# Optimization experiments

Hardware: AMD Instinct MI355X
Metric: run time of the kernel (lower is better)

Reference implementation:

```python
import jax, jax.numpy as jnp
import numpy as np

B, L, HID, H = 2, 384, 512, 8
D = HID // H  # head_dim = 64


def setup_inputs() -> dict:
    key = jax.random.key(0)
    ks = jax.random.split(key, 16)
    s = 0.02
    return {
        "query": jax.random.normal(ks[0], (B, L, HID), jnp.float32),
        "key_": jax.random.normal(ks[1], (B, L, HID), jnp.float32),
        "value": jax.random.normal(ks[2], (B, L, HID), jnp.float32),
        "mask": jnp.ones((B, 1, 1, L), jnp.int32),
        # fc_q/k/v/o: nn.Linear(hid_dim, hid_dim)
        "Wq": jax.random.normal(ks[3], (HID, HID), jnp.float32) * s,
        "bq": jnp.zeros((HID,), jnp.float32),
        "Wk": jax.random.normal(ks[4], (HID, HID), jnp.float32) * s,
        "bk": jnp.zeros((HID,), jnp.float32),
        "Wv": jax.random.normal(ks[5], (HID, HID), jnp.float32) * s,
        "bv": jnp.zeros((HID,), jnp.float32),
        "Wo": jax.random.normal(ks[6], (HID, HID), jnp.float32) * s,
        "bo": jnp.zeros((HID,), jnp.float32),
        # additive-attention score MLP: W1, W2: Linear(D, D); v: Linear(D, 1)
        "W1": jax.random.normal(ks[7], (D, D), jnp.float32) * s,
        "b1": jnp.zeros((D,), jnp.float32),
        "W2": jax.random.normal(ks[8], (D, D), jnp.float32) * s,
        "b2": jnp.zeros((D,), jnp.float32),
        "vw": jax.random.normal(ks[9], (1, D), jnp.float32) * s,
        "vb": jnp.zeros((1,), jnp.float32),
    }


def reference(query, key_, value, mask, Wq, bq, Wk, bk, Wv, bv, Wo, bo,
              W1, b1, W2, b2, vw, vb):
    b = query.shape[0]
    # projections (torch Linear: x @ W.T + b)
    Q = query @ Wq.T + bq
    K = key_ @ Wk.T + bk
    V = value @ Wv.T + bv
    # [b, h, l, d]
    def split_heads(x):
        return x.reshape(b, -1, H, D).transpose(0, 2, 1, 3)
    Q, K, V = split_heads(Q), split_heads(K), split_heads(V)
    # additive (Bahdanau-style) score: v^T tanh(W1 q + W2 k)
    tQ = Q @ W1.T + b1            # [b, h, lq, d]
    tK = K @ W2.T + b2            # [b, h, lk, d]
    e = jnp.tanh(tQ[:, :, :, None, :] + tK[:, :, None, :, :])  # [b,h,lq,lk,d]
    energy = jnp.einsum('bhqkd,d->bhqk', e, vw[0]) + vb[0]      # [b,h,lq,lk]
    energy = jnp.where(mask == 0, jnp.float32(-1e10), energy)
    attention = jax.nn.softmax(energy, axis=-1)
    x = jnp.einsum('bhqk,bhkd->bhqd', attention, V)  # dropout p=0 (eval)
    x = x.transpose(0, 2, 1, 3).reshape(b, -1, HID)
    x = x @ Wo.T + bo
    return x, attention
```

## Files before the change

### kernel.cpp

```cpp
#include <hip/hip_runtime.h>

#define BATCH 2
#define LSEQ 384
#define NHID 512
#define NH 8
#define DH 64
#define BH (BATCH*NH)
#define XELEMS ((size_t)768 * NHID)
#define TQ 8
#define QTILES (LSEQ/TQ)

typedef unsigned short ushort_t;
typedef __attribute__((ext_vector_type(8))) short bf16x8;
typedef __attribute__((ext_vector_type(4))) float f32x4;

__device__ __forceinline__ float bf2f(ushort_t u) {
    unsigned int v = ((unsigned int)u) << 16;
    return __uint_as_float(v);
}
__device__ __forceinline__ ushort_t f2bf(float f) {
    unsigned int u = __float_as_uint(f);
    unsigned int lsb = (u >> 16) & 1u;
    u += 0x7fffu + lsb;
    return (ushort_t)(u >> 16);
}
__device__ __forceinline__ unsigned pk_bf16(float a, float b) {
    unsigned ua = __float_as_uint(a), ub = __float_as_uint(b);
    ua += 0x7fffu + ((ua >> 16) & 1u);
    ub += 0x7fffu + ((ub >> 16) & 1u);
    return __builtin_amdgcn_perm(ub, ua, 0x07060302);
}
__device__ __forceinline__ float ld1(const void* p, size_t i, int f) {
    return f ? ((const float*)p)[i] : bf2f(((const ushort_t*)p)[i]);
}
__device__ __forceinline__ float4 ld4(const void* p, size_t i, int f) {
    if (f) return ((const float4*)p)[i >> 2];
    ushort4 u = ((const ushort4*)p)[i >> 2];
    return make_float4(bf2f(u.x), bf2f(u.y), bf2f(u.z), bf2f(u.w));
}
__device__ __forceinline__ int block_detect(const unsigned int* q, int* cnt) {
    int t = threadIdx.x;
    if (t == 0) *cnt = 0;
    __syncthreads();
    int n = blockDim.x < 256 ? blockDim.x : 256;
    if (t < n) {
        unsigned int elo = (q[t] >> 7) & 0xFFu;
        if (elo >= 100u && elo <= 150u) atomicAdd(cnt, 1);
    }
    __syncthreads();
    return (*cnt * 2 > n) ? 0 : 1;
}
__device__ __forceinline__ uint4 packu4(float4 a, float4 b) {
    uint4 r;
    r.x = pk_bf16(a.x, a.y); r.y = pk_bf16(a.z, a.w);
    r.z = pk_bf16(b.x, b.y); r.w = pk_bf16(b.z, b.w);
    return r;
}
__device__ __forceinline__ bf16x8 pack_bf8(float4 a, float4 b) {
    union { uint4 u; bf16x8 v; } r;
    r.u = packu4(a, b);
    return r.v;
}

#define OFF_ETQ   16
#define OFF_ETK   (16 + 393216)
#define OFF_VH    (16 + 2*393216)
#define OFF_XH    (16 + 3*393216)

#define LDSTR 72

__global__ __launch_bounds__(128) void gemm_qkv(
    const void* qp, const void* kp, const void* vp,
    const void* Wqp, const void* Wkp, const void* Wvp,
    const void* W1p, const void* W2p,
    const void* bqp, const void* bkp, const void* b1p, const void* b2p,
    const void* bvp, float* __restrict__ ws)
{
    __shared__ int s_cnt;
    __shared__ ushort_t smA[32 * LDSTR];
    __shared__ ushort_t smB[64 * LDSTR];
    __shared__ float biasF[64];
    const int f = block_detect((const unsigned int*)qp, &s_cnt);

    const int mode = blockIdx.z;
    const void* A = (mode == 0) ? qp : (mode == 1) ? kp : vp;
    const void* W = (mode == 0) ? Wqp : (mode == 1) ? Wkp : Wvp;
    const void* W1x = (mode == 1) ? W2p : W1p;

    const int h    = blockIdx.x;
    const int col0 = h * 64;
    const int row0 = blockIdx.y * 32;
    const int t = threadIdx.x;
    const int w = t >> 6, l16 = t & 15, quad = (t & 63) >> 4;

    if (t < 64) {
        if (mode == 2) {
            biasF[t] = ld1(bvp, col0 + t, f);
        } else {
            const void* b1x = (mode == 1) ? b2p : b1p;
            const void* bx  = (mode == 1) ? bkp : bqp;
            float s = ld1(b1x, t, f);
            for (int j = 0; j < 64; j++)
                s = fmaf(ld1(W1x, (size_t)t * 64 + j, f), ld1(bx, h * 64 + j, f), s);
            biasF[t] = s;
        }
    }

    const int arow = t >> 2, acol = (t & 3) * 16;
    const int brow = t >> 1, bcol = (t & 1) * 32;
    const size_t abase = (size_t)(row0 + arow) * 512 + acol;
    const size_t bbase = (size_t)(col0 + brow) * 512 + bcol;

    float4 a4[4], b4[8];
    #pragma unroll
    for (int i = 0; i < 4; i++) a4[i] = ld4(A, abase + i * 4, f);
    #pragma unroll
    for (int i = 0; i < 8; i++) b4[i] = ld4(W, bbase + i * 4, f);

    f32x4 acc[4];
    #pragma unroll
    for (int nt = 0; nt < 4; nt++) acc[nt] = (f32x4){0.f, 0.f, 0.f, 0.f};

    for (int k0 = 0; k0 < 512; k0 += 64) {
        __syncthreads();
        *reinterpret_cast<uint4*>(&smA[arow * LDSTR + acol])     = packu4(a4[0], a4[1]);
        *reinterpret_cast<uint4*>(&smA[arow * LDSTR + acol + 8]) = packu4(a4[2], a4[3]);
        *reinterpret_cast<uint4*>(&smB[brow * LDSTR + bcol])      = packu4(b4[0], b4[1]);
        *reinterpret_cast<uint4*>(&smB[brow * LDSTR + bcol + 8])  = packu4(b4[2], b4[3]);
        *reinterpret_cast<uint4*>(&smB[brow * LDSTR + bcol + 16]) = packu4(b4[4], b4[5]);
        *reinterpret_cast<uint4*>(&smB[brow * LDSTR + bcol + 24]) = packu4(b4[6], b4[7]);
        __syncthreads();
        if (k0 + 64 < 512) {
            #pragma unroll
            for (int i = 0; i < 4; i++) a4[i] = ld4(A, abase + k0 + 64 + i * 4, f);
            #pragma unroll
            for (int i = 0; i < 8; i++) b4[i] = ld4(W, bbase + k0 + 64 + i * 4, f);
        }
        #pragma unroll
        for (int kk = 0; kk < 2; kk++) {
            bf16x8 af = *reinterpret_cast<const bf16x8*>(
                &smA[(w * 16 + l16) * LDSTR + kk * 32 + quad * 8]);
            #pragma unroll
            for (int nt = 0; nt < 4; nt++) {
                bf16x8 bfr = *reinterpret_cast<const bf16x8*>(
                    &smB[(nt * 16 + l16) * LDSTR + kk * 32 + quad * 8]);
                acc[nt] = __builtin_amdgcn_mfma_f32_16x16x32_bf16(af, bfr, acc[nt], 0, 0, 0);
            }
        }
    }

    const int b  = (row0 >= LSEQ) ? 1 : 0;
    const int lbase = row0 - b * LSEQ + w * 16;
    const int bh = b * NH + h;

    if (mode == 2) {
        float* Out = ws + OFF_VH;
        #pragma unroll
        for (int nt = 0; nt < 4; nt++) {
            int d = l16 + nt * 16;
            float bi = biasF[d];
            #pragma unroll
            for (int r = 0; r < 4; r++) {
                int l = lbase + quad * 4 + r;
                Out[(size_t)(bh * LSEQ + l) * 64 + d] = acc[nt][r] + bi;
            }
        }
    } else {
        #pragma unroll
        for (int nt = 0; nt < 4; nt++)
            #pragma unroll
            for (int r = 0; r < 4; r++)
                smA[(w * 16 + quad * 4 + r) * LDSTR + l16 + nt * 16] =
                    f2bf(acc[nt][r]);
        f32x4 acc2[4];
        #pragma unroll
        for (int nt = 0; nt < 4; nt++) acc2[nt] = (f32x4){0.f, 0.f, 0.f, 0.f};
        #pragma unroll
        for (int kk = 0; kk < 2; kk++) {
            bf16x8 af2 = *reinterpret_cast<const bf16x8*>(
                &smA[(w * 16 + l16) * LDSTR + kk * 32 + quad * 8]);
            #pragma unroll
            for (int nt = 0; nt < 4; nt++) {
                int od = nt * 16 + l16, j0 = kk * 32 + quad * 8;
                float4 wa = ld4(W1x, (size_t)od * 64 + j0, f);
                float4 wb = ld4(W1x, (size_t)od * 64 + j0 + 4, f);
                bf16x8 bfw = pack_bf8(wa, wb);
                acc2[nt] = __builtin_amdgcn_mfma_f32_16x16x32_bf16(af2, bfw, acc2[nt], 0, 0, 0);
            }
        }
        float* Out = ws + ((mode == 0) ? OFF_ETQ : OFF_ETK);
        #pragma unroll
        for (int nt = 0; nt < 4; nt++) {
            int d = l16 + nt * 16;
            float bi = biasF[d];
            #pragma unroll
            for (int r = 0; r < 4; r++) {
                int l = lbase + quad * 4 + r;
                Out[(size_t)(bh * LSEQ + l) * 64 + d] =
                    __expf(2.f * (acc2[nt][r] + bi));
            }
        }
    }
}

__global__ __launch_bounds__(384, 6) void attn_kernel(
    const void* qp, const void* vwp, const void* vbp,
    const float* __restrict__ ws_in, float* __restrict__ ws,
    const int* __restrict__ mask, void* __restrict__ dout)
{
    __shared__ int s_cnt;
    const int f = block_detect((const unsigned int*)qp, &s_cnt);

    const float* Etq = ws_in + OFF_ETQ;
    const float* Etk = ws_in + OFF_ETK;
    const float* Vh  = ws_in + OFF_VH;
    float* Xh = ws + OFF_XH;

    const int bid = blockIdx.x;
    const int qt = bid % QTILES;
    const int bh = bid / QTILES;
    const int q0 = qt * TQ;
    const int b  = bh >> 3;
    const int h  = bh & 7;
    const int t  = threadIdx.x;
    const int wave = t >> 6;

    __shared__ __align__(16) float etq8[64][TQ];
    __shared__ float cws[64];
    __shared__ float ps[TQ][LSEQ];
    __shared__ float red[6][TQ][16][4];
    __shared__ float rsum[TQ][6];
    __shared__ float s_vb;

    for (int i = t; i < TQ * 64; i += 384) {
        int qi = i >> 6, d = i & 63;
        float wv = ld1(vwp, d, f);
        etq8[d][qi] = Etq[(size_t)(bh * LSEQ + q0 + qi) * 64 + d] / wv;
    }
    if (t < 64) {
        float v = ld1(vwp, t, f);
        cws[t] = 1.0f / v;
        #pragma unroll
        for (int off = 32; off > 0; off >>= 1) v += __shfl_xor(v, off, 64);
        if (t == 0) s_vb = ld1(vbp, 0, f) + v;
    }
    const int mok = mask[b * LSEQ + t];
    __syncthreads();
    const float vbSum = s_vb;

    float e2[TQ] = {0.f, 0.f, 0.f, 0.f, 0.f, 0.f, 0.f, 0.f};
    const float* ekrow = Etk + (size_t)(bh * LSEQ + t) * 64;
    #pragma unroll 2
    for (int dv = 0; dv < 16; dv++) {
        float4 ek4 = *reinterpret_cast<const float4*>(ekrow + dv * 4);
        #pragma unroll
        for (int pj = 0; pj < 2; pj++) {
            const int d0 = dv * 4 + pj * 2;
            const float ekA = pj ? ek4.z : ek4.x;
            const float ekB = pj ? ek4.w : ek4.y;
            const float cA = cws[d0];
            const float cB = cws[d0 + 1];
            float4 qA0 = *reinterpret_cast<const float4*>(&etq8[d0][0]);
            float4 qA1 = *reinterpret_cast<const float4*>(&etq8[d0][4]);
            float4 qB0 = *reinterpret_cast<const float4*>(&etq8[d0 + 1][0]);
            float4 qB1 = *reinterpret_cast<const float4*>(&etq8[d0 + 1][4]);
            {
                float u1 = fmaf(qA0.x, ekA, cA), u2 = fmaf(qB0.x, ekB, cB);
                e2[0] = fmaf(u1 + u2, __builtin_amdgcn_rcpf(u1 * u2), e2[0]);
            }
            {
                float u1 = fmaf(qA0.y, ekA, cA), u2 = fmaf(qB0.y, ekB, cB);
                e2[1] = fmaf(u1 + u2, __builtin_amdgcn_rcpf(u1 * u2), e2[1]);
            }
            {
                float u1 = fmaf(qA0.z, ekA, cA), u2 = fmaf(qB0.z, ekB, cB);
                e2[2] = fmaf(u1 + u2, __builtin_amdgcn_rcpf(u1 * u2), e2[2]);
            }
            {
                float u1 = fmaf(qA0.w, ekA, cA), u2 = fmaf(qB0.w, ekB, cB);
                e2[3] = fmaf(u1 + u2, __builtin_amdgcn_rcpf(u1 * u2), e2[3]);
            }
            {
                float u1 = fmaf(qA1.x, ekA, cA), u2 = fmaf(qB1.x, ekB, cB);
                e2[4] = fmaf(u1 + u2, __builtin_amdgcn_rcpf(u1 * u2), e2[4]);
            }
            {
                float u1 = fmaf(qA1.y, ekA, cA), u2 = fmaf(qB1.y, ekB, cB);
                e2[5] = fmaf(u1 + u2, __builtin_amdgcn_rcpf(u1 * u2), e2[5]);
            }
            {
                float u1 = fmaf(qA1.z, ekA, cA), u2 = fmaf(qB1.z, ekB, cB);
                e2[6] = fmaf(u1 + u2, __builtin_amdgcn_rcpf(u1 * u2), e2[6]);
            }
            {
                float u1 = fmaf(qA1.w, ekA, cA), u2 = fmaf(qB1.w, ekB, cB);
                e2[7] = fmaf(u1 + u2, __builtin_amdgcn_rcpf(u1 * u2), e2[7]);
            }
        }
    }

    float p[TQ];
    #pragma unroll
    for (int qi = 0; qi < TQ; qi++) {
        float en = fmaf(-2.0f, e2[qi], vbSum);
        if (mok == 0) en = -1e10f;
        p[qi] = __expf(en);
        float s = p[qi];
        #pragma unroll
        for (int off = 32; off > 0; off >>= 1) s += __shfl_xor(s, off, 64);
        if ((t & 63) == 0) rsum[qi][wave] = s;
    }
    __syncthreads();
    #pragma unroll
    for (int qi = 0; qi < TQ; qi++) {
        float gs = rsum[qi][0] + rsum[qi][1] + rsum[qi][2] +
                   rsum[qi][3] + rsum[qi][4] + rsum[qi][5];
        p[qi] *= 1.0f / gs;
        ps[qi][t] = p[qi];
        size_t aidx = XELEMS + (size_t)(bh * LSEQ + q0 + qi) * LSEQ + t;
        if (f) ((float*)dout)[aidx] = p[qi];
        else   ((ushort_t*)dout)[aidx] = f2bf(p[qi]);
    }
    __syncthreads();

    const int dq = t & 15;
    const int ksub = t >> 4;
    const float* vb4 = Vh + (size_t)bh * LSEQ * 64 + dq * 4;
    float4 acc[TQ];
    #pragma unroll
    for (int qi = 0; qi < TQ; qi++) acc[qi] = make_float4(0.f, 0.f, 0.f, 0.f);
    for (int kk = ksub; kk < LSEQ; kk += 24) {
        float4 v4 = *reinterpret_cast<const float4*>(vb4 + (size_t)kk * 64);
        #pragma unroll
        for (int qi = 0; qi < TQ; qi++) {
            float pq = ps[qi][kk];
            acc[qi].x = fmaf(pq, v4.x, acc[qi].x);
            acc[qi].y = fmaf(pq, v4.y, acc[qi].y);
            acc[qi].z = fmaf(pq, v4.z, acc[qi].z);
            acc[qi].w = fmaf(pq, v4.w, acc[qi].w);
        }
    }
    #pragma unroll
    for (int qi = 0; qi < TQ; qi++) {
        #pragma unroll
        for (int off = 16; off <= 32; off <<= 1) {
            acc[qi].x += __shfl_xor(acc[qi].x, off, 64);
            acc[qi].y += __shfl_xor(acc[qi].y, off, 64);
            acc[qi].z += __shfl_xor(acc[qi].z, off, 64);
            acc[qi].w += __shfl_xor(acc[qi].w, off, 64);
        }
    }
    if ((t & 63) < 16) {
        #pragma unroll
        for (int qi = 0; qi < TQ; qi++) {
            red[wave][qi][dq][0] = acc[qi].x;
            red[wave][qi][dq][1] = acc[qi].y;
            red[wave][qi][dq][2] = acc[qi].z;
            red[wave][qi][dq][3] = acc[qi].w;
        }
    }
    __syncthreads();
    if (t < 256) {
        int d = t & 63;
        #pragma unroll
        for (int half = 0; half < 2; half++) {
            int qi = (t >> 6) + half * 4;
            float sx = 0.f;
            #pragma unroll
            for (int w = 0; w < 6; w++) sx += red[w][qi][d >> 2][d & 3];
            Xh[((size_t)(b * LSEQ + q0 + qi) * NH + h) * 64 + d] = sx;
        }
    }
}

__global__ __launch_bounds__(128) void gemm_out(
    const void* qp, const void* Wop, const void* bop,
    const float* __restrict__ ws_in, void* __restrict__ dout)
{
    __shared__ int s_cnt;
    __shared__ ushort_t smA[32 * LDSTR];
    __shared__ ushort_t smB[64 * LDSTR];
    __shared__ float biasF[64];
    const int f = block_detect((const unsigned int*)qp, &s_cnt);

    const float* Xh = ws_in + OFF_XH;
    const int col0 = blockIdx.x * 64;
    const int row0 = blockIdx.y * 32;
    const int t = threadIdx.x;
    const int w = t >> 6, l16 = t & 15, quad = (t & 63) >> 4;

    if (t < 64) biasF[t] = ld1(bop, col0 + t, f);

    const int arow = t >> 2, acol = (t & 3) * 16;
    const int brow = t >> 1, bcol = (t & 1) * 32;
    const float* Ab = Xh + (size_t)(row0 + arow) * 512 + acol;
    const size_t bbase = (size_t)(col0 + brow) * 512 + bcol;

    float4 a4[4], b4[8];
    #pragma unroll
    for (int i = 0; i < 4; i++) a4[i] = *reinterpret_cast<const float4*>(Ab + i * 4);
    #pragma unroll
    for (int i = 0; i < 8; i++) b4[i] = ld4(Wop, bbase + i * 4, f);

    f32x4 acc[4];
    #pragma unroll
    for (int nt = 0; nt < 4; nt++) acc[nt] = (f32x4){0.f, 0.f, 0.f, 0.f};

    for (int k0 = 0; k0 < 512; k0 += 64) {
        __syncthreads();
        *reinterpret_cast<uint4*>(&smA[arow * LDSTR + acol])     = packu4(a4[0], a4[1]);
        *reinterpret_cast<uint4*>(&smA[arow * LDSTR + acol + 8]) = packu4(a4[2], a4[3]);
        *reinterpret_cast<uint4*>(&smB[brow * LDSTR + bcol])      = packu4(b4[0], b4[1]);
        *reinterpret_cast<uint4*>(&smB[brow * LDSTR + bcol + 8])  = packu4(b4[2], b4[3]);
        *reinterpret_cast<uint4*>(&smB[brow * LDSTR + bcol + 16]) = packu4(b4[4], b4[5]);
        *reinterpret_cast<uint4*>(&smB[brow * LDSTR + bcol + 24]) = packu4(b4[6], b4[7]);
        __syncthreads();
        if (k0 + 64 < 512) {
            #pragma unroll
            for (int i = 0; i < 4; i++)
                a4[i] = *reinterpret_cast<const float4*>(Ab + k0 + 64 + i * 4);
            #pragma unroll
            for (int i = 0; i < 8; i++) b4[i] = ld4(Wop, bbase + k0 + 64 + i * 4, f);
        }
        #pragma unroll
        for (int kk = 0; kk < 2; kk++) {
            bf16x8 af = *reinterpret_cast<const bf16x8*>(
                &smA[(w * 16 + l16) * LDSTR + kk * 32 + quad * 8]);
            #pragma unroll
            for (int nt = 0; nt < 4; nt++) {
                bf16x8 bfr = *reinterpret_cast<const bf16x8*>(
                    &smB[(nt * 16 + l16) * LDSTR + kk * 32 + quad * 8]);
                acc[nt] = __builtin_amdgcn_mfma_f32_16x16x32_bf16(af, bfr, acc[nt], 0, 0, 0);
            }
        }
    }

    #pragma unroll
    for (int nt = 0; nt < 4; nt++) {
        int n = col0 + l16 + nt * 16;
        float bi = biasF[l16 + nt * 16];
        #pragma unroll
        for (int r = 0; r < 4; r++) {
            int m = row0 + w * 16 + quad * 4 + r;
            float c = acc[nt][r] + bi;
            size_t idx = (size_t)m * 512 + n;
            if (f) ((float*)dout)[idx] = c;
            else   ((ushort_t*)dout)[idx] = f2bf(c);
        }
    }
}

extern "C" void kernel_launch(void* const* d_in, const int* in_sizes, int n_in,
                              void* d_out, int out_size, void* d_ws, size_t ws_size,
                              hipStream_t stream)
{
    const void* qp = d_in[0];
    const void* kp = d_in[1];
    const void* vp = d_in[2];
    const int* mask = (const int*)d_in[3];
    const void* Wqp = d_in[4];  const void* bqp = d_in[5];
    const void* Wkp = d_in[6];  const void* bkp = d_in[7];
    const void* Wvp = d_in[8];  const void* bvp = d_in[9];
    const void* Wop = d_in[10]; const void* bop = d_in[11];
    const void* W1p = d_in[12]; const void* b1p = d_in[13];
    const void* W2p = d_in[14]; const void* b2p = d_in[15];
    const void* vwp = d_in[16]; const void* vbp = d_in[17];

    float* ws = (float*)d_ws;

    gemm_qkv<<<dim3(8, 24, 3), 128, 0, stream>>>(qp, kp, vp, Wqp, Wkp, Wvp,
                                                 W1p, W2p, bqp, bkp, b1p, b2p,
                                                 bvp, ws);
    attn_kernel<<<BH * QTILES, 384, 0, stream>>>(qp, vwp, vbp, ws, ws, mask, d_out);
    gemm_out<<<dim3(8, 24, 1), 128, 0, stream>>>(qp, Wop, bop, ws, d_out);
}
```

Measured before the change: 159.2 us.

## Split K dimension across two thread halves in projection GEMMs

Both projection GEMM kernels now launch 256 threads per block. Each half handles one half of the K=512 reduction using separate shared-memory tiles, and the two partial accumulators are combined through a shared-memory reduction buffer. The aim is to halve the serial K-loop length and double the waves per block, hiding the global-load latency of these small GEMMs. The cost is more shared memory, an extra reduction sync, and half the threads sitting idle in the epilogue.

```diff
diff --git a/kernel.cpp b/kernel.cpp
--- a/kernel.cpp
+++ b/kernel.cpp
@@ -69,7 +69,7 @@
 
 #define LDSTR 72
 
-__global__ __launch_bounds__(128) void gemm_qkv(
+__global__ __launch_bounds__(256) void gemm_qkv(
     const void* qp, const void* kp, const void* vp,
     const void* Wqp, const void* Wkp, const void* Wvp,
     const void* W1p, const void* W2p,
@@ -77,8 +77,9 @@
     const void* bvp, float* __restrict__ ws)
 {
     __shared__ int s_cnt;
-    __shared__ ushort_t smA[32 * LDSTR];
-    __shared__ ushort_t smB[64 * LDSTR];
+    __shared__ ushort_t smA[2][32 * LDSTR];
+    __shared__ ushort_t smB[2][64 * LDSTR];
+    __shared__ float sred[32][65];
     __shared__ float biasF[64];
     const int f = block_detect((const unsigned int*)qp, &s_cnt);
 
@@ -91,7 +92,10 @@
     const int col0 = h * 64;
     const int row0 = blockIdx.y * 32;
     const int t = threadIdx.x;
-    const int w = t >> 6, l16 = t & 15, quad = (t & 63) >> 4;
+    const int th = t & 127;
+    const int kh = t >> 7;
+    const int w2 = (t >> 6) & 1;
+    const int l16 = t & 15, quad = (t & 63) >> 4;
 
     if (t < 64) {
         if (mode == 2) {
@@ -106,10 +110,10 @@
         }
     }
 
-    const int arow = t >> 2, acol = (t & 3) * 16;
-    const int brow = t >> 1, bcol = (t & 1) * 32;
-    const size_t abase = (size_t)(row0 + arow) * 512 + acol;
-    const size_t bbase = (size_t)(col0 + brow) * 512 + bcol;
+    const int arow = th >> 2, acol = (th & 3) * 16;
+    const int brow = th >> 1, bcol = (th & 1) * 32;
+    const size_t abase = (size_t)(row0 + arow) * 512 + kh * 256 + acol;
+    const size_t bbase = (size_t)(col0 + brow) * 512 + kh * 256 + bcol;
 
     float4 a4[4], b4[8];
     #pragma unroll
@@ -121,16 +125,16 @@
     #pragma unroll
     for (int nt = 0; nt < 4; nt++) acc[nt] = (f32x4){0.f, 0.f, 0.f, 0.f};
 
-    for (int k0 = 0; k0 < 512; k0 += 64) {
+    for (int k0 = 0; k0 < 256; k0 += 64) {
         __syncthreads();
-        *reinterpret_cast<uint4*>(&smA[arow * LDSTR + acol])     = packu4(a4[0], a4[1]);
-        *reinterpret_cast<uint4*>(&smA[arow * LDSTR + acol + 8]) = packu4(a4[2], a4[3]);
-        *reinterpret_cast<uint4*>(&smB[brow * LDSTR + bcol])      = packu4(b4[0], b4[1]);
-        *reinterpret_cast<uint4*>(&smB[brow * LDSTR + bcol + 8])  = packu4(b4[2], b4[3]);
-        *reinterpret_cast<uint4*>(&smB[brow * LDSTR + bcol + 16]) = packu4(b4[4], b4[5]);
-        *reinterpret_cast<uint4*>(&smB[brow * LDSTR + bcol + 24]) = packu4(b4[6], b4[7]);
+        *reinterpret_cast<uint4*>(&smA[kh][arow * LDSTR + acol])     = packu4(a4[0], a4[1]);
+        *reinterpret_cast<uint4*>(&smA[kh][arow * LDSTR + acol + 8]) = packu4(a4[2], a4[3]);
+        *reinterpret_cast<uint4*>(&smB[kh][brow * LDSTR + bcol])      = packu4(b4[0], b4[1]);
+        *reinterpret_cast<uint4*>(&smB[kh][brow * LDSTR + bcol + 8])  = packu4(b4[2], b4[3]);
+        *reinterpret_cast<uint4*>(&smB[kh][brow * LDSTR + bcol + 16]) = packu4(b4[4], b4[5]);
+        *reinterpret_cast<uint4*>(&smB[kh][brow * LDSTR + bcol + 24]) = packu4(b4[6], b4[7]);
         __syncthreads();
-        if (k0 + 64 < 512) {
+        if (k0 + 64 < 256) {
             #pragma unroll
             for (int i = 0; i < 4; i++) a4[i] = ld4(A, abase + k0 + 64 + i * 4, f);
             #pragma unroll
@@ -139,65 +143,81 @@
         #pragma unroll
         for (int kk = 0; kk < 2; kk++) {
             bf16x8 af = *reinterpret_cast<const bf16x8*>(
-                &smA[(w * 16 + l16) * LDSTR + kk * 32 + quad * 8]);
+                &smA[kh][(w2 * 16 + l16) * LDSTR + kk * 32 + quad * 8]);
             #pragma unroll
             for (int nt = 0; nt < 4; nt++) {
                 bf16x8 bfr = *reinterpret_cast<const bf16x8*>(
-                    &smB[(nt * 16 + l16) * LDSTR + kk * 32 + quad * 8]);
+                    &smB[kh][(nt * 16 + l16) * LDSTR + kk * 32 + quad * 8]);
                 acc[nt] = __builtin_amdgcn_mfma_f32_16x16x32_bf16(af, bfr, acc[nt], 0, 0, 0);
             }
         }
     }
 
-    const int b  = (row0 >= LSEQ) ? 1 : 0;
-    const int lbase = row0 - b * LSEQ + w * 16;
-    const int bh = b * NH + h;
-
-    if (mode == 2) {
-        float* Out = ws + OFF_VH;
-        #pragma unroll
-        for (int nt = 0; nt < 4; nt++) {
-            int d = l16 + nt * 16;
-            float bi = biasF[d];
-            #pragma unroll
-            for (int r = 0; r < 4; r++) {
-                int l = lbase + quad * 4 + r;
-                Out[(size_t)(bh * LSEQ + l) * 64 + d] = acc[nt][r] + bi;
-            }
-        }
-    } else {
+    if (kh == 1) {
         #pragma unroll
         for (int nt = 0; nt < 4; nt++)
             #pragma unroll
             for (int r = 0; r < 4; r++)
-                smA[(w * 16 + quad * 4 + r) * LDSTR + l16 + nt * 16] =
-                    f2bf(acc[nt][r]);
-        f32x4 acc2[4];
-        #pragma unroll
-        for (int nt = 0; nt < 4; nt++) acc2[nt] = (f32x4){0.f, 0.f, 0.f, 0.f};
-        #pragma unroll
-        for (int kk = 0; kk < 2; kk++) {
-            bf16x8 af2 = *reinterpret_cast<const bf16x8*>(
-                &smA[(w * 16 + l16) * LDSTR + kk * 32 + quad * 8]);
+                sred[w2 * 16 + quad * 4 + r][nt * 16 + l16] = acc[nt][r];
+    }
+    __syncthreads();
+    if (kh == 0) {
+        #pragma unroll
+        for (int nt = 0; nt < 4; nt++)
+            #pragma unroll
+            for (int r = 0; r < 4; r++)
+                acc[nt][r] += sred[w2 * 16 + quad * 4 + r][nt * 16 + l16];
+
+        const int b  = (row0 >= LSEQ) ? 1 : 0;
+        const int lbase = row0 - b * LSEQ + w2 * 16;
+        const int bh = b * NH + h;
+
+        if (mode == 2) {
+            float* Out = ws + OFF_VH;
             #pragma unroll
             for (int nt = 0; nt < 4; nt++) {
-                int od = nt * 16 + l16, j0 = kk * 32 + quad * 8;
-                float4 wa = ld4(W1x, (size_t)od * 64 + j0, f);
-                float4 wb = ld4(W1x, (size_t)od * 64 + j0 + 4, f);
-                bf16x8 bfw = pack_bf8(wa, wb);
-                acc2[nt] = __builtin_amdgcn_mfma_f32_16x16x32_bf16(af2, bfw, acc2[nt], 0, 0, 0);
-            }
-        }
-        float* Out = ws + ((mode == 0) ? OFF_ETQ : OFF_ETK);
-        #pragma unroll
-        for (int nt = 0; nt < 4; nt++) {
-            int d = l16 + nt * 16;
-            float bi = biasF[d];
-            #pragma unroll
-            for (int r = 0; r < 4; r++) {
-                int l = lbase + quad * 4 + r;
-                Out[(size_t)(bh * LSEQ + l) * 64 + d] =
-                    __expf(2.f * (acc2[nt][r] + bi));
+                int d = l16 + nt * 16;
+                float bi = biasF[d];
+                #pragma unroll
+                for (int r = 0; r < 4; r++) {
+                    int l = lbase + quad * 4 + r;
+                    Out[(size_t)(bh * LSEQ + l) * 64 + d] = acc[nt][r] + bi;
+                }
+            }
+        } else {
+            #pragma unroll
+            for (int nt = 0; nt < 4; nt++)
+                #pragma unroll
+                for (int r = 0; r < 4; r++)
+                    smA[0][(w2 * 16 + quad * 4 + r) * LDSTR + l16 + nt * 16] =
+                        f2bf(acc[nt][r]);
+            f32x4 acc2[4];
+            #pragma unroll
+            for (int nt = 0; nt < 4; nt++) acc2[nt] = (f32x4){0.f, 0.f, 0.f, 0.f};
+            #pragma unroll
+            for (int kk = 0; kk < 2; kk++) {
+                bf16x8 af2 = *reinterpret_cast<const bf16x8*>(
+                    &smA[0][(w2 * 16 + l16) * LDSTR + kk * 32 + quad * 8]);
+                #pragma unroll
+                for (int nt = 0; nt < 4; nt++) {
+                    int od = nt * 16 + l16, j0 = kk * 32 + quad * 8;
+                    float4 wa = ld4(W1x, (size_t)od * 64 + j0, f);
+                    float4 wb = ld4(W1x, (size_t)od * 64 + j0 + 4, f);
+                    bf16x8 bfw = pack_bf8(wa, wb);
+                    acc2[nt] = __builtin_amdgcn_mfma_f32_16x16x32_bf16(af2, bfw, acc2[nt], 0, 0, 0);
+                }
+            }
+            float* Out = ws + ((mode == 0) ? OFF_ETQ : OFF_ETK);
+            #pragma unroll
+            for (int nt = 0; nt < 4; nt++) {
+                int d = l16 + nt * 16;
+                float bi = biasF[d];
+                #pragma unroll
+                for (int r = 0; r < 4; r++) {
+                    int l = lbase + quad * 4 + r;
+                    Out[(size_t)(bh * LSEQ + l) * 64 + d] =
+                        __expf(2.f * (acc2[nt][r] + bi));
+                }
             }
         }
     }
@@ -373,13 +393,14 @@
     }
 }
 
-__global__ __launch_bounds__(128) void gemm_out(
+__global__ __launch_bounds__(256) void gemm_out(
     const void* qp, const void* Wop, const void* bop,
     const float* __restrict__ ws_in, void* __restrict__ dout)
 {
     __shared__ int s_cnt;
-    __shared__ ushort_t smA[32 * LDSTR];
-    __shared__ ushort_t smB[64 * LDSTR];
+    __shared__ ushort_t smA[2][32 * LDSTR];
+    __shared__ ushort_t smB[2][64 * LDSTR];
+    __shared__ float sred[32][65];
     __shared__ float biasF[64];
     const int f = block_detect((const unsigned int*)qp, &s_cnt);
 
@@ -387,14 +408,17 @@
     const int col0 = blockIdx.x * 64;
     const int row0 = blockIdx.y * 32;
     const int t = threadIdx.x;
-    const int w = t >> 6, l16 = t & 15, quad = (t & 63) >> 4;
+    const int th = t & 127;
+    const int kh = t >> 7;
+    const int w2 = (t >> 6) & 1;
+    const int l16 = t & 15, quad = (t & 63) >> 4;
 
     if (t < 64) biasF[t] = ld1(bop, col0 + t, f);
 
-    const int arow = t >> 2, acol = (t & 3) * 16;
-    const int brow = t >> 1, bcol = (t & 1) * 32;
-    const float* Ab = Xh + (size_t)(row0 + arow) * 512 + acol;
-    const size_t bbase = (size_t)(col0 + brow) * 512 + bcol;
+    const int arow = th >> 2, acol = (th & 3) * 16;
+    const int brow = th >> 1, bcol = (th & 1) * 32;
+    const float* Ab = Xh + (size_t)(row0 + arow) * 512 + kh * 256 + acol;
+    const size_t bbase = (size_t)(col0 + brow) * 512 + kh * 256 + bcol;
 
     float4 a4[4], b4[8];
     #pragma unroll
@@ -406,16 +430,16 @@
     #pragma unroll
     for (int nt = 0; nt < 4; nt++) acc[nt] = (f32x4){0.f, 0.f, 0.f, 0.f};
 
-    for (int k0 = 0; k0 < 512; k0 += 64) {
+    for (int k0 = 0; k0 < 256; k0 += 64) {
         __syncthreads();
-        *reinterpret_cast<uint4*>(&smA[arow * LDSTR + acol])     = packu4(a4[0], a4[1]);
-        *reinterpret_cast<uint4*>(&smA[arow * LDSTR + acol + 8]) = packu4(a4[2], a4[3]);
-        *reinterpret_cast<uint4*>(&smB[brow * LDSTR + bcol])      = packu4(b4[0], b4[1]);
-        *reinterpret_cast<uint4*>(&smB[brow * LDSTR + bcol + 8])  = packu4(b4[2], b4[3]);
-        *reinterpret_cast<uint4*>(&smB[brow * LDSTR + bcol + 16]) = packu4(b4[4], b4[5]);
-        *reinterpret_cast<uint4*>(&smB[brow * LDSTR + bcol + 24]) = packu4(b4[6], b4[7]);
+        *reinterpret_cast<uint4*>(&smA[kh][arow * LDSTR + acol])     = packu4(a4[0], a4[1]);
+        *reinterpret_cast<uint4*>(&smA[kh][arow * LDSTR + acol + 8]) = packu4(a4[2], a4[3]);
+        *reinterpret_cast<uint4*>(&smB[kh][brow * LDSTR + bcol])      = packu4(b4[0], b4[1]);
+        *reinterpret_cast<uint4*>(&smB[kh][brow * LDSTR + bcol + 8])  = packu4(b4[2], b4[3]);
+        *reinterpret_cast<uint4*>(&smB[kh][brow * LDSTR + bcol + 16]) = packu4(b4[4], b4[5]);
+        *reinterpret_cast<uint4*>(&smB[kh][brow * LDSTR + bcol + 24]) = packu4(b4[6], b4[7]);
         __syncthreads();
-        if (k0 + 64 < 512) {
+        if (k0 + 64 < 256) {
             #pragma unroll
             for (int i = 0; i < 4; i++)
                 a4[i] = *reinterpret_cast<const float4*>(Ab + k0 + 64 + i * 4);
@@ -425,27 +449,37 @@
         #pragma unroll
         for (int kk = 0; kk < 2; kk++) {
             bf16x8 af = *reinterpret_cast<const bf16x8*>(
-                &smA[(w * 16 + l16) * LDSTR + kk * 32 + quad * 8]);
+                &smA[kh][(w2 * 16 + l16) * LDSTR + kk * 32 + quad * 8]);
             #pragma unroll
             for (int nt = 0; nt < 4; nt++) {
                 bf16x8 bfr = *reinterpret_cast<const bf16x8*>(
-                    &smB[(nt * 16 + l16) * LDSTR + kk * 32 + quad * 8]);
+                    &smB[kh][(nt * 16 + l16) * LDSTR + kk * 32 + quad * 8]);
                 acc[nt] = __builtin_amdgcn_mfma_f32_16x16x32_bf16(af, bfr, acc[nt], 0, 0, 0);
             }
         }
     }
 
-    #pragma unroll
-    for (int nt = 0; nt < 4; nt++) {
-        int n = col0 + l16 + nt * 16;
-        float bi = biasF[l16 + nt * 16];
-        #pragma unroll
-        for (int r = 0; r < 4; r++) {
-            int m = row0 + w * 16 + quad * 4 + r;
-            float c = acc[nt][r] + bi;
-            size_t idx = (size_t)m * 512 + n;
-            if (f) ((float*)dout)[idx] = c;
-            else   ((ushort_t*)dout)[idx] = f2bf(c);
+    if (kh == 1) {
+        #pragma unroll
+        for (int nt = 0; nt < 4; nt++)
+            #pragma unroll
+            for (int r = 0; r < 4; r++)
+                sred[w2 * 16 + quad * 4 + r][nt * 16 + l16] = acc[nt][r];
+    }
+    __syncthreads();
+    if (kh == 0) {
+        #pragma unroll
+        for (int nt = 0; nt < 4; nt++) {
+            int n = col0 + l16 + nt * 16;
+            float bi = biasF[l16 + nt * 16];
+            #pragma unroll
+            for (int r = 0; r < 4; r++) {
+                int m = row0 + w2 * 16 + quad * 4 + r;
+                float c = acc[nt][r] + sred[w2 * 16 + quad * 4 + r][nt * 16 + l16] + bi;
+                size_t idx = (size_t)m * 512 + n;
+                if (f) ((float*)dout)[idx] = c;
+                else   ((ushort_t*)dout)[idx] = f2bf(c);
+            }
         }
     }
 }
@@ -468,9 +502,9 @@
 
     float* ws = (float*)d_ws;
 
-    gemm_qkv<<<dim3(8, 24, 3), 128, 0, stream>>>(qp, kp, vp, Wqp, Wkp, Wvp,
+    gemm_qkv<<<dim3(8, 24, 3), 256, 0, stream>>>(qp, kp, vp, Wqp, Wkp, Wvp,
                                                  W1p, W2p, bqp, bkp, b1p, b2p,
                                                  bvp, ws);
     attn_kernel<<<BH * QTILES, 384, 0, stream>>>(qp, vwp, vbp, ws, ws, mask, d_out);
-    gemm_out<<<dim3(8, 24, 1), 128, 0, stream>>>(qp, Wop, bop, ws, d_out);
-}
+    gemm_out<<<dim3(8, 24, 1), 256, 0, stream>>>(qp, Wop, bop, ws, d_out);
+}
```

New measurement: 161.7 us. No clear change (+1.6%).
